# Kernel optimization log

Hardware: AMD Instinct MI355X
Metric: run time of the kernel (lower is better)

The kernel has to match this reference:

```python
import jax, jax.numpy as jnp
import numpy as np


def setup_inputs() -> dict:
    key = jax.random.key(0)
    kq, kk, kv = jax.random.split(key, 3)
    B, S, H, HK, D = 2, 2048, 32, 8, 128
    q = jax.random.normal(kq, (B, S, H, D), dtype=jnp.float32)
    k = jax.random.normal(kk, (B, S, HK, D), dtype=jnp.float32)
    v = jax.random.normal(kv, (B, S, HK, D), dtype=jnp.float32)
    return {"q": q, "k": k, "v": v}


def reference(q, k, v):
    # Causal grouped-query attention (the math vLLM's paged attention computes
    # for a full prefill where the KV cache holds exactly this sequence).
    B, S, H, D = q.shape
    HK = k.shape[2]
    G = H // HK  # query heads per kv head
    scale = jnp.asarray(D, q.dtype) ** -0.5
    qg = q.reshape(B, S, HK, G, D)
    # scores: [B, HK, G, S(q), S(k)]
    scores = jnp.einsum("bshgd,bthd->bhgst", qg, k) * scale
    causal = jnp.tril(jnp.ones((S, S), dtype=bool))  # [Sq, Sk]
    scores = jnp.where(causal, scores, jnp.finfo(scores.dtype).min)
    probs = jax.nn.softmax(scores, axis=-1)
    out = jnp.einsum("bhgst,bthd->bshgd", probs, v)  # [B, S, HK, G, D]
    return out.reshape(B, S, H * D)
```

## Files before the change

kernel.cpp:

```cpp
#include <hip/hip_runtime.h>
#include <hip/hip_bf16.h>

typedef __attribute__((ext_vector_type(8))) short short8;
typedef __attribute__((ext_vector_type(4))) short short4v;
typedef __attribute__((ext_vector_type(4))) float f32x4;
typedef __attribute__((ext_vector_type(16))) float f32x16;

#define MFMA32(a,b,c) __builtin_amdgcn_mfma_f32_32x32x16_bf16(a,b,c,0,0,0)

static __device__ __forceinline__ short f2bf(float f){
    union{float f;unsigned u;}x; x.f=f;
    unsigned r=(x.u+0x7FFFu+((x.u>>16)&1u))>>16;
    return (short)r;
}

static __device__ __forceinline__ unsigned pkbf(float lo, float hi){
    unsigned r;
    asm("v_cvt_pk_bf16_f32 %0, %1, %2" : "=v"(r) : "v"(lo), "v"(hi));
    return r;
}

static __device__ __forceinline__ void gl_lds16(const void* g, void* l){
    __builtin_amdgcn_global_load_lds(
        (const __attribute__((address_space(1))) unsigned int*)g,
        (__attribute__((address_space(3))) unsigned int*)l, 16, 0, 0);
}

static __device__ __forceinline__ short8 pfrag(int hi,
        float e0,float e1,float e2,float e3,
        float e4,float e5,float e6,float e7){
    unsigned a01 = pkbf(e0,e1), a23 = pkbf(e2,e3);
    unsigned a45 = pkbf(e4,e5), a67 = pkbf(e6,e7);
    unsigned b01 = __shfl_xor(a01, 32);
    unsigned b23 = __shfl_xor(a23, 32);
    unsigned b45 = __shfl_xor(a45, 32);
    unsigned b67 = __shfl_xor(a67, 32);
    union{ unsigned u[4]; short8 s; } w;
    w.u[0] = hi ? b45 : a01;
    w.u[1] = hi ? b67 : a23;
    w.u[2] = hi ? a45 : b01;
    w.u[3] = hi ? a67 : b23;
    return w.s;
}

constexpr int S_=2048, H_=32, HK_=8, D_=128;
constexpr int KVBLK=64;

__global__ __launch_bounds__(256) void prep_k(const float* __restrict__ k, short* __restrict__ kb){
    int t = blockIdx.x*256 + threadIdx.x;
    int e = t*4;
    int d  = e & 127;
    int hk = (e>>7) & 7;
    int s  = (e>>10) & 2047;
    int b  = e>>21;
    f32x4 x = *(const f32x4*)(k + ((size_t)((b*S_+s)*HK_+hk))*D_ + d);
    short4v o;
    o[0]=f2bf(x[0]); o[1]=f2bf(x[1]); o[2]=f2bf(x[2]); o[3]=f2bf(x[3]);
    *(short4v*)(kb + ((size_t)((b*HK_+hk)*S_+s))*D_ + d) = o;
}

__global__ __launch_bounds__(256) void prep_vt(const float* __restrict__ v, short* __restrict__ vt){
    __shared__ short tile[64*65];
    int bid = blockIdx.x;
    int d0 = (bid & 1)*64;
    int s0 = ((bid>>1) & 31)*64;
    int hk = (bid>>6) & 7;
    int b  = bid>>9;
    int tid = threadIdx.x;
    #pragma unroll
    for(int i=0;i<4;i++){
        int idx = i*1024 + tid*4;
        int r = idx>>6, c = idx&63;
        f32x4 x = *(const f32x4*)(v + ((size_t)((b*S_+s0+r)*HK_+hk))*D_ + d0 + c);
        tile[(c+0)*65 + r] = f2bf(x[0]);
        tile[(c+1)*65 + r] = f2bf(x[1]);
        tile[(c+2)*65 + r] = f2bf(x[2]);
        tile[(c+3)*65 + r] = f2bf(x[3]);
    }
    __syncthreads();
    #pragma unroll
    for(int i=0;i<4;i++){
        int idx = i*1024 + tid*4;
        int dr = idx>>6, c = idx&63;
        short4v o;
        o[0]=tile[dr*65+c]; o[1]=tile[dr*65+c+1]; o[2]=tile[dr*65+c+2]; o[3]=tile[dr*65+c+3];
        *(short4v*)(vt + ((size_t)((b*HK_+hk)*D_ + d0+dr))*S_ + s0 + c) = o;
    }
}

__global__ __launch_bounds__(512,2) void attn_fwd(
    const float* __restrict__ q, const short* __restrict__ kb,
    const short* __restrict__ vtb, float* __restrict__ out)
{
    __shared__ __align__(16) unsigned char kls[2][KVBLK*D_*2];
    __shared__ __align__(16) unsigned char vls[2][D_*KVBLK*2];

    const int bid  = blockIdx.x;
    const int qt   = 7 - (bid >> 6);
    const int head = bid & 63;
    const int b    = head >> 5;
    const int h    = head & 31;
    const int hk   = h >> 2;
    const int q0   = qt * 256;

    const int tid  = threadIdx.x;
    const int wave = tid >> 6;
    const int ln   = tid & 31;
    const int hi   = (tid >> 5) & 1;
    const int qg   = q0 + wave*32 + ln;

    const float qscale = 0.08838834764831845f * 1.4426950408889634f;

    const short* kt_base = kb  + (size_t)(b*HK_+hk)*S_*D_;
    const short* vt_base = vtb + (size_t)(b*HK_+hk)*D_*S_;

    short8 qf[8];
    {
        const float* qp = q + ((size_t)(b*S_ + qg)*H_ + h)*D_;
        #pragma unroll
        for(int kk=0;kk<8;kk++){
            int d0 = kk*16 + hi*8;
            f32x4 a = *(const f32x4*)(qp + d0);
            f32x4 c = *(const f32x4*)(qp + d0 + 4);
            union{ unsigned u[4]; short8 s; } w;
            w.u[0]=pkbf(a[0]*qscale, a[1]*qscale);
            w.u[1]=pkbf(a[2]*qscale, a[3]*qscale);
            w.u[2]=pkbf(c[0]*qscale, c[1]*qscale);
            w.u[3]=pkbf(c[2]*qscale, c[3]*qscale);
            qf[kk]=w.s;
        }
    }

    f32x16 oac[4];
    #pragma unroll
    for(int dt=0;dt<4;dt++) oac[dt] = (f32x16)0.f;
    float m = -1e30f, l = 0.f;

    auto STAGE = [&](int bufi, int kvt){
        const char* kg = (const char*)(kt_base + (size_t)kvt*KVBLK*D_);
        #pragma unroll
        for(int i=0;i<2;i++){
            int p = (i*512 + tid)*16;
            int src = p ^ (((p>>8)&7)<<4);
            gl_lds16(kg + src, &kls[bufi][p]);
        }
        const char* vg = (const char*)vt_base + (size_t)kvt*KVBLK*2;
        #pragma unroll
        for(int i=0;i<2;i++){
            int p = (i*512 + tid)*16;
            int d = p>>7;
            int src = (p&127) ^ ((d&7)<<4);
            gl_lds16(vg + (size_t)d*(S_*2) + src, &vls[bufi][p]);
        }
    };

    const int nkv     = q0/64 + 4;
    const int kvmax_w = (q0 + wave*32 + 31) >> 6;

    STAGE(0, 0);
    __syncthreads();
    int cur = 0;

    for(int kvt=0; kvt<nkv; ++kvt){
        if (kvt+1 < nkv) STAGE(cur^1, kvt+1);

        if (kvt <= kvmax_w){
            const int kv0 = kvt*64;
            f32x16 sa0=(f32x16)0.f, sa1=(f32x16)0.f;
            const int sz = (ln&7)<<4;
            #pragma unroll
            for(int kk=0;kk<8;kk++){
                int c = kk*32 + hi*16;
                short8 k0 = *(const short8*)&kls[cur][(ln*256 + c) ^ sz];
                short8 k1 = *(const short8*)&kls[cur][((ln+32)*256 + c) ^ sz];
                sa0 = MFMA32(k0, qf[kk], sa0);
                sa1 = MFMA32(k1, qf[kk], sa1);
            }
            if (kv0 + 63 > q0 + wave*32){
                #pragma unroll
                for(int r=0;r<16;r++){
                    int kvl = (r&3) + 8*(r>>2) + 4*hi;
                    if (kv0 + kvl      > qg) sa0[r] = -1e30f;
                    if (kv0 + 32 + kvl > qg) sa1[r] = -1e30f;
                }
            }
            float pm = sa0[0];
            #pragma unroll
            for(int r=1;r<16;r++) pm = fmaxf(pm, sa0[r]);
            #pragma unroll
            for(int r=0;r<16;r++) pm = fmaxf(pm, sa1[r]);
            pm = fmaxf(pm, __shfl_xor(pm, 32));
            float mn = fmaxf(m, pm);
            float sf = __builtin_amdgcn_exp2f(m - mn);
            m = mn;
            float ps = 0.f;
            #pragma unroll
            for(int r=0;r<16;r++){ sa0[r] = __builtin_amdgcn_exp2f(sa0[r]-mn); ps += sa0[r]; }
            #pragma unroll
            for(int r=0;r<16;r++){ sa1[r] = __builtin_amdgcn_exp2f(sa1[r]-mn); ps += sa1[r]; }
            l = l*sf + (ps + __shfl_xor(ps, 32));
            #pragma unroll
            for(int dt=0;dt<4;dt++){
                #pragma unroll
                for(int r=0;r<16;r++) oac[dt][r] *= sf;
            }
            short8 pa0 = pfrag(hi, sa0[0],sa0[1],sa0[2], sa0[3], sa0[4], sa0[5], sa0[6], sa0[7]);
            short8 pa1 = pfrag(hi, sa0[8],sa0[9],sa0[10],sa0[11],sa0[12],sa0[13],sa0[14],sa0[15]);
            short8 pa2 = pfrag(hi, sa1[0],sa1[1],sa1[2], sa1[3], sa1[4], sa1[5], sa1[6], sa1[7]);
            short8 pa3 = pfrag(hi, sa1[8],sa1[9],sa1[10],sa1[11],sa1[12],sa1[13],sa1[14],sa1[15]);
            #pragma unroll
            for(int dt=0;dt<4;dt++){
                int rb = (dt*32 + ln)*128;
                short8 v0 = *(const short8*)&vls[cur][(rb +   0 + hi*16) ^ sz];
                oac[dt] = MFMA32(v0, pa0, oac[dt]);
                short8 v1 = *(const short8*)&vls[cur][(rb +  32 + hi*16) ^ sz];
                oac[dt] = MFMA32(v1, pa1, oac[dt]);
                short8 v2 = *(const short8*)&vls[cur][(rb +  64 + hi*16) ^ sz];
                oac[dt] = MFMA32(v2, pa2, oac[dt]);
                short8 v3 = *(const short8*)&vls[cur][(rb +  96 + hi*16) ^ sz];
                oac[dt] = MFMA32(v3, pa3, oac[dt]);
            }
        }
        __syncthreads();
        cur ^= 1;
    }

    float rinv = 1.0f / l;
    float* op = out + ((size_t)(b*S_ + qg)*H_ + h)*D_;
    #pragma unroll
    for(int dt=0;dt<4;dt++){
        #pragma unroll
        for(int rr=0;rr<4;rr++){
            f32x4 o4;
            o4[0]=oac[dt][rr*4+0]*rinv;
            o4[1]=oac[dt][rr*4+1]*rinv;
            o4[2]=oac[dt][rr*4+2]*rinv;
            o4[3]=oac[dt][rr*4+3]*rinv;
            *(f32x4*)(op + dt*32 + rr*8 + hi*4) = o4;
        }
    }
}

extern "C" void kernel_launch(void* const* d_in, const int* in_sizes, int n_in,
                              void* d_out, int out_size, void* d_ws, size_t ws_size,
                              hipStream_t stream) {
    const float* q = (const float*)d_in[0];
    const float* k = (const float*)d_in[1];
    const float* v = (const float*)d_in[2];
    float* out = (float*)d_out;

    short* kb = (short*)d_ws;
    short* vt = (short*)((char*)d_ws + (size_t)2*HK_*S_*D_*2);

    prep_k <<<dim3(4096), dim3(256), 0, stream>>>(k, kb);
    prep_vt<<<dim3(1024), dim3(256), 0, stream>>>(v, vt);

    attn_fwd<<<dim3(512), dim3(512), 0, stream>>>(q, kb, vt, out);
}
```

Measured before the change: 120.6 us.

## Pair causal q-tiles per workgroup, merge prep kernels, add lazy rescale and setprio

```diff
diff --git a/kernel.cpp b/kernel.cpp
--- a/kernel.cpp
+++ b/kernel.cpp
@@ -46,49 +46,51 @@
 constexpr int S_=2048, H_=32, HK_=8, D_=128;
 constexpr int KVBLK=64;
 
-__global__ __launch_bounds__(256) void prep_k(const float* __restrict__ k, short* __restrict__ kb){
-    int t = blockIdx.x*256 + threadIdx.x;
-    int e = t*4;
-    int d  = e & 127;
-    int hk = (e>>7) & 7;
-    int s  = (e>>10) & 2047;
-    int b  = e>>21;
-    f32x4 x = *(const f32x4*)(k + ((size_t)((b*S_+s)*HK_+hk))*D_ + d);
-    short4v o;
-    o[0]=f2bf(x[0]); o[1]=f2bf(x[1]); o[2]=f2bf(x[2]); o[3]=f2bf(x[3]);
-    *(short4v*)(kb + ((size_t)((b*HK_+hk)*S_+s))*D_ + d) = o;
-}
-
-__global__ __launch_bounds__(256) void prep_vt(const float* __restrict__ v, short* __restrict__ vt){
+__global__ __launch_bounds__(256) void prep(const float* __restrict__ k, const float* __restrict__ v,
+                                            short* __restrict__ kb, short* __restrict__ vt){
     __shared__ short tile[64*65];
     int bid = blockIdx.x;
-    int d0 = (bid & 1)*64;
-    int s0 = ((bid>>1) & 31)*64;
-    int hk = (bid>>6) & 7;
-    int b  = bid>>9;
-    int tid = threadIdx.x;
-    #pragma unroll
-    for(int i=0;i<4;i++){
-        int idx = i*1024 + tid*4;
-        int r = idx>>6, c = idx&63;
-        f32x4 x = *(const f32x4*)(v + ((size_t)((b*S_+s0+r)*HK_+hk))*D_ + d0 + c);
-        tile[(c+0)*65 + r] = f2bf(x[0]);
-        tile[(c+1)*65 + r] = f2bf(x[1]);
-        tile[(c+2)*65 + r] = f2bf(x[2]);
-        tile[(c+3)*65 + r] = f2bf(x[3]);
+    if (bid < 4096){
+        int t = bid*256 + threadIdx.x;
+        int e = t*4;
+        int d  = e & 127;
+        int hk = (e>>7) & 7;
+        int s  = (e>>10) & 2047;
+        int b  = e>>21;
+        f32x4 x = *(const f32x4*)(k + ((size_t)((b*S_+s)*HK_+hk))*D_ + d);
+        short4v o;
+        o[0]=f2bf(x[0]); o[1]=f2bf(x[1]); o[2]=f2bf(x[2]); o[3]=f2bf(x[3]);
+        *(short4v*)(kb + ((size_t)((b*HK_+hk)*S_+s))*D_ + d) = o;
+    } else {
+        bid -= 4096;
+        int d0 = (bid & 1)*64;
+        int s0 = ((bid>>1) & 31)*64;
+        int hk = (bid>>6) & 7;
+        int b  = bid>>9;
+        int tid = threadIdx.x;
+        #pragma unroll
+        for(int i=0;i<4;i++){
+            int idx = i*1024 + tid*4;
+            int r = idx>>6, c = idx&63;
+            f32x4 x = *(const f32x4*)(v + ((size_t)((b*S_+s0+r)*HK_+hk))*D_ + d0 + c);
+            tile[(c+0)*65 + r] = f2bf(x[0]);
+            tile[(c+1)*65 + r] = f2bf(x[1]);
+            tile[(c+2)*65 + r] = f2bf(x[2]);
+            tile[(c+3)*65 + r] = f2bf(x[3]);
+        }
+        __syncthreads();
+        #pragma unroll
+        for(int i=0;i<4;i++){
+            int idx = i*1024 + tid*4;
+            int dr = idx>>6, c = idx&63;
+            short4v o;
+            o[0]=tile[dr*65+c]; o[1]=tile[dr*65+c+1]; o[2]=tile[dr*65+c+2]; o[3]=tile[dr*65+c+3];
+            *(short4v*)(vt + ((size_t)((b*HK_+hk)*D_ + d0+dr))*S_ + s0 + c) = o;
+        }
     }
-    __syncthreads();
-    #pragma unroll
-    for(int i=0;i<4;i++){
-        int idx = i*1024 + tid*4;
-        int dr = idx>>6, c = idx&63;
-        short4v o;
-        o[0]=tile[dr*65+c]; o[1]=tile[dr*65+c+1]; o[2]=tile[dr*65+c+2]; o[3]=tile[dr*65+c+3];
-        *(short4v*)(vt + ((size_t)((b*HK_+hk)*D_ + d0+dr))*S_ + s0 + c) = o;
-    }
-}
-
-__global__ __launch_bounds__(512,2) void attn_fwd(
+}
+
+__global__ __launch_bounds__(256,2) void attn_fwd(
     const float* __restrict__ q, const short* __restrict__ kb,
     const short* __restrict__ vtb, float* __restrict__ out)
 {
@@ -96,147 +98,158 @@
     __shared__ __align__(16) unsigned char vls[2][D_*KVBLK*2];
 
     const int bid  = blockIdx.x;
-    const int qt   = 7 - (bid >> 6);
-    const int head = bid & 63;
-    const int b    = head >> 5;
-    const int h    = head & 31;
-    const int hk   = h >> 2;
-    const int q0   = qt * 256;
+    const int wg   = (bid & 7)*64 + (bid >> 3);
+    const int kvg  = wg >> 5;
+    const int b    = kvg >> 3;
+    const int hk   = kvg & 7;
+    const int rr_  = wg & 31;
+    const int h    = hk*4 + (rr_ >> 3);
+    const int pair = rr_ & 7;
 
     const int tid  = threadIdx.x;
     const int wave = tid >> 6;
     const int ln   = tid & 31;
     const int hi   = (tid >> 5) & 1;
-    const int qg   = q0 + wave*32 + ln;
 
     const float qscale = 0.08838834764831845f * 1.4426950408889634f;
 
     const short* kt_base = kb  + (size_t)(b*HK_+hk)*S_*D_;
     const short* vt_base = vtb + (size_t)(b*HK_+hk)*D_*S_;
 
-    short8 qf[8];
-    {
-        const float* qp = q + ((size_t)(b*S_ + qg)*H_ + h)*D_;
-        #pragma unroll
-        for(int kk=0;kk<8;kk++){
-            int d0 = kk*16 + hi*8;
-            f32x4 a = *(const f32x4*)(qp + d0);
-            f32x4 c = *(const f32x4*)(qp + d0 + 4);
-            union{ unsigned u[4]; short8 s; } w;
-            w.u[0]=pkbf(a[0]*qscale, a[1]*qscale);
-            w.u[1]=pkbf(a[2]*qscale, a[3]*qscale);
-            w.u[2]=pkbf(c[0]*qscale, c[1]*qscale);
-            w.u[3]=pkbf(c[2]*qscale, c[3]*qscale);
-            qf[kk]=w.s;
-        }
-    }
-
-    f32x16 oac[4];
-    #pragma unroll
-    for(int dt=0;dt<4;dt++) oac[dt] = (f32x16)0.f;
-    float m = -1e30f, l = 0.f;
-
     auto STAGE = [&](int bufi, int kvt){
         const char* kg = (const char*)(kt_base + (size_t)kvt*KVBLK*D_);
         #pragma unroll
-        for(int i=0;i<2;i++){
-            int p = (i*512 + tid)*16;
+        for(int i=0;i<4;i++){
+            int p = (i*256 + tid)*16;
             int src = p ^ (((p>>8)&7)<<4);
             gl_lds16(kg + src, &kls[bufi][p]);
         }
         const char* vg = (const char*)vt_base + (size_t)kvt*KVBLK*2;
         #pragma unroll
-        for(int i=0;i<2;i++){
-            int p = (i*512 + tid)*16;
+        for(int i=0;i<4;i++){
+            int p = (i*256 + tid)*16;
             int d = p>>7;
             int src = (p&127) ^ ((d&7)<<4);
             gl_lds16(vg + (size_t)d*(S_*2) + src, &vls[bufi][p]);
         }
     };
 
-    const int nkv     = q0/64 + 4;
-    const int kvmax_w = (q0 + wave*32 + 31) >> 6;
-
+    int cur = 0;
     STAGE(0, 0);
     __syncthreads();
-    int cur = 0;
-
-    for(int kvt=0; kvt<nkv; ++kvt){
-        if (kvt+1 < nkv) STAGE(cur^1, kvt+1);
-
-        if (kvt <= kvmax_w){
-            const int kv0 = kvt*64;
-            f32x16 sa0=(f32x16)0.f, sa1=(f32x16)0.f;
-            const int sz = (ln&7)<<4;
+
+    for(int phase=0; phase<2; ++phase){
+        const int c      = phase ? pair : 15-pair;
+        const int nkv    = 2*c + 2;
+        const int kvmaxw = 2*c + (wave >> 1);
+        const int qg     = c*128 + wave*32 + ln;
+
+        short8 qf[8];
+        {
+            const float* qp = q + ((size_t)(b*S_ + qg)*H_ + h)*D_;
             #pragma unroll
             for(int kk=0;kk<8;kk++){
-                int c = kk*32 + hi*16;
-                short8 k0 = *(const short8*)&kls[cur][(ln*256 + c) ^ sz];
-                short8 k1 = *(const short8*)&kls[cur][((ln+32)*256 + c) ^ sz];
-                sa0 = MFMA32(k0, qf[kk], sa0);
-                sa1 = MFMA32(k1, qf[kk], sa1);
+                int d0 = kk*16 + hi*8;
+                f32x4 a = *(const f32x4*)(qp + d0);
+                f32x4 cc= *(const f32x4*)(qp + d0 + 4);
+                union{ unsigned u[4]; short8 s; } w;
+                w.u[0]=pkbf(a[0]*qscale, a[1]*qscale);
+                w.u[1]=pkbf(a[2]*qscale, a[3]*qscale);
+                w.u[2]=pkbf(cc[0]*qscale, cc[1]*qscale);
+                w.u[3]=pkbf(cc[2]*qscale, cc[3]*qscale);
+                qf[kk]=w.s;
             }
-            if (kv0 + 63 > q0 + wave*32){
-                #pragma unroll
-                for(int r=0;r<16;r++){
-                    int kvl = (r&3) + 8*(r>>2) + 4*hi;
-                    if (kv0 + kvl      > qg) sa0[r] = -1e30f;
-                    if (kv0 + 32 + kvl > qg) sa1[r] = -1e30f;
-                }
+        }
+
+        f32x16 oac[4];
+        #pragma unroll
+        for(int dt=0;dt<4;dt++) oac[dt] = (f32x16)0.f;
+        float m = -1e30f, l = 0.f;
+
+        for(int kvt=0; kvt<nkv; ++kvt){
+            int nxt = (kvt+1 < nkv) ? (kvt+1) : (phase==0 ? 0 : -1);
+            if (nxt >= 0) STAGE(cur^1, nxt);
+
+            if (kvt <= kvmaxw){
+                const int kv0 = kvt*64;
+                f32x16 sa0=(f32x16)0.f, sa1=(f32x16)0.f;
+                const int sz = (ln&7)<<4;
+                __builtin_amdgcn_s_setprio(1);
+                #pragma unroll
+                for(int kk=0;kk<8;kk++){
+                    int cb = kk*32 + hi*16;
+                    short8 k0 = *(const short8*)&kls[cur][(ln*256 + cb) ^ sz];
+                    short8 k1 = *(const short8*)&kls[cur][((ln+32)*256 + cb) ^ sz];
+                    sa0 = MFMA32(k0, qf[kk], sa0);
+                    sa1 = MFMA32(k1, qf[kk], sa1);
+                }
+                __builtin_amdgcn_s_setprio(0);
+                if (kv0 + 63 > c*128 + wave*32){
+                    #pragma unroll
+                    for(int r=0;r<16;r++){
+                        int kvl = (r&3) + 8*(r>>2) + 4*hi;
+                        if (kv0 + kvl      > qg) sa0[r] = -1e30f;
+                        if (kv0 + 32 + kvl > qg) sa1[r] = -1e30f;
+                    }
+                }
+                float pm = sa0[0];
+                #pragma unroll
+                for(int r=1;r<16;r++) pm = fmaxf(pm, sa0[r]);
+                #pragma unroll
+                for(int r=0;r<16;r++) pm = fmaxf(pm, sa1[r]);
+                pm = fmaxf(pm, __shfl_xor(pm, 32));
+                if (!__all(pm <= m + 8.f)){
+                    float mn = fmaxf(m, pm);
+                    float sf = __builtin_amdgcn_exp2f(m - mn);
+                    m = mn; l *= sf;
+                    #pragma unroll
+                    for(int dt=0;dt<4;dt++){
+                        #pragma unroll
+                        for(int r=0;r<16;r++) oac[dt][r] *= sf;
+                    }
+                }
+                float ps = 0.f;
+                #pragma unroll
+                for(int r=0;r<16;r++){ sa0[r] = __builtin_amdgcn_exp2f(sa0[r]-m); ps += sa0[r]; }
+                #pragma unroll
+                for(int r=0;r<16;r++){ sa1[r] = __builtin_amdgcn_exp2f(sa1[r]-m); ps += sa1[r]; }
+                l += ps + __shfl_xor(ps, 32);
+                short8 pa0 = pfrag(hi, sa0[0],sa0[1],sa0[2], sa0[3], sa0[4], sa0[5], sa0[6], sa0[7]);
+                short8 pa1 = pfrag(hi, sa0[8],sa0[9],sa0[10],sa0[11],sa0[12],sa0[13],sa0[14],sa0[15]);
+                short8 pa2 = pfrag(hi, sa1[0],sa1[1],sa1[2], sa1[3], sa1[4], sa1[5], sa1[6], sa1[7]);
+                short8 pa3 = pfrag(hi, sa1[8],sa1[9],sa1[10],sa1[11],sa1[12],sa1[13],sa1[14],sa1[15]);
+                __builtin_amdgcn_s_setprio(1);
+                #pragma unroll
+                for(int dt=0;dt<4;dt++){
+                    int rb = (dt*32 + ln)*128;
+                    short8 v0 = *(const short8*)&vls[cur][(rb +   0 + hi*16) ^ sz];
+                    oac[dt] = MFMA32(v0, pa0, oac[dt]);
+                    short8 v1 = *(const short8*)&vls[cur][(rb +  32 + hi*16) ^ sz];
+                    oac[dt] = MFMA32(v1, pa1, oac[dt]);
+                    short8 v2 = *(const short8*)&vls[cur][(rb +  64 + hi*16) ^ sz];
+                    oac[dt] = MFMA32(v2, pa2, oac[dt]);
+                    short8 v3 = *(const short8*)&vls[cur][(rb +  96 + hi*16) ^ sz];
+                    oac[dt] = MFMA32(v3, pa3, oac[dt]);
+                }
+                __builtin_amdgcn_s_setprio(0);
             }
-            float pm = sa0[0];
+            __syncthreads();
+            cur ^= 1;
+        }
+
+        float rinv = 1.0f / l;
+        float* op = out + ((size_t)(b*S_ + qg)*H_ + h)*D_;
+        #pragma unroll
+        for(int dt=0;dt<4;dt++){
             #pragma unroll
-            for(int r=1;r<16;r++) pm = fmaxf(pm, sa0[r]);
-            #pragma unroll
-            for(int r=0;r<16;r++) pm = fmaxf(pm, sa1[r]);
-            pm = fmaxf(pm, __shfl_xor(pm, 32));
-            float mn = fmaxf(m, pm);
-            float sf = __builtin_amdgcn_exp2f(m - mn);
-            m = mn;
-            float ps = 0.f;
-            #pragma unroll
-            for(int r=0;r<16;r++){ sa0[r] = __builtin_amdgcn_exp2f(sa0[r]-mn); ps += sa0[r]; }
-            #pragma unroll
-            for(int r=0;r<16;r++){ sa1[r] = __builtin_amdgcn_exp2f(sa1[r]-mn); ps += sa1[r]; }
-            l = l*sf + (ps + __shfl_xor(ps, 32));
-            #pragma unroll
-            for(int dt=0;dt<4;dt++){
-                #pragma unroll
-                for(int r=0;r<16;r++) oac[dt][r] *= sf;
+            for(int rr=0;rr<4;rr++){
+                f32x4 o4;
+                o4[0]=oac[dt][rr*4+0]*rinv;
+                o4[1]=oac[dt][rr*4+1]*rinv;
+                o4[2]=oac[dt][rr*4+2]*rinv;
+                o4[3]=oac[dt][rr*4+3]*rinv;
+                *(f32x4*)(op + dt*32 + rr*8 + hi*4) = o4;
             }
-            short8 pa0 = pfrag(hi, sa0[0],sa0[1],sa0[2], sa0[3], sa0[4], sa0[5], sa0[6], sa0[7]);
-            short8 pa1 = pfrag(hi, sa0[8],sa0[9],sa0[10],sa0[11],sa0[12],sa0[13],sa0[14],sa0[15]);
-            short8 pa2 = pfrag(hi, sa1[0],sa1[1],sa1[2], sa1[3], sa1[4], sa1[5], sa1[6], sa1[7]);
-            short8 pa3 = pfrag(hi, sa1[8],sa1[9],sa1[10],sa1[11],sa1[12],sa1[13],sa1[14],sa1[15]);
-            #pragma unroll
-            for(int dt=0;dt<4;dt++){
-                int rb = (dt*32 + ln)*128;
-                short8 v0 = *(const short8*)&vls[cur][(rb +   0 + hi*16) ^ sz];
-                oac[dt] = MFMA32(v0, pa0, oac[dt]);
-                short8 v1 = *(const short8*)&vls[cur][(rb +  32 + hi*16) ^ sz];
-                oac[dt] = MFMA32(v1, pa1, oac[dt]);
-                short8 v2 = *(const short8*)&vls[cur][(rb +  64 + hi*16) ^ sz];
-                oac[dt] = MFMA32(v2, pa2, oac[dt]);
-                short8 v3 = *(const short8*)&vls[cur][(rb +  96 + hi*16) ^ sz];
-                oac[dt] = MFMA32(v3, pa3, oac[dt]);
-            }
-        }
-        __syncthreads();
-        cur ^= 1;
-    }
-
-    float rinv = 1.0f / l;
-    float* op = out + ((size_t)(b*S_ + qg)*H_ + h)*D_;
-    #pragma unroll
-    for(int dt=0;dt<4;dt++){
-        #pragma unroll
-        for(int rr=0;rr<4;rr++){
-            f32x4 o4;
-            o4[0]=oac[dt][rr*4+0]*rinv;
-            o4[1]=oac[dt][rr*4+1]*rinv;
-            o4[2]=oac[dt][rr*4+2]*rinv;
-            o4[3]=oac[dt][rr*4+3]*rinv;
-            *(f32x4*)(op + dt*32 + rr*8 + hi*4) = o4;
         }
     }
 }
@@ -252,8 +265,6 @@
     short* kb = (short*)d_ws;
     short* vt = (short*)((char*)d_ws + (size_t)2*HK_*S_*D_*2);
 
-    prep_k <<<dim3(4096), dim3(256), 0, stream>>>(k, kb);
-    prep_vt<<<dim3(1024), dim3(256), 0, stream>>>(v, vt);
-
-    attn_fwd<<<dim3(512), dim3(512), 0, stream>>>(q, kb, vt, out);
-}
+    prep<<<dim3(4096+1024), dim3(256), 0, stream>>>(k, v, kb, vt);
+    attn_fwd<<<dim3(512), dim3(256), 0, stream>>>(q, kb, vt, out);
+}
```

Result: faster. 116.5 us (-3.4%).
